# Optimization experiments

Measured on AMD Instinct MI355X. Metric: run time of the kernel, lower is better.

Reference implementation:

```python
import jax, jax.numpy as jnp
import numpy as np


def setup_inputs() -> dict:
    key = jax.random.key(0)
    kx, kw = jax.random.split(key)
    x = jax.random.normal(kx, (32, 2048, 256), dtype=jnp.float32)
    W = jax.random.normal(kw, (1024, 256), dtype=jnp.float32)  # codebook [K, D]
    return {"x": x, "W": W}


def reference(x, W):
    D = W.shape[1]
    flat = x.reshape(-1, D)  # [N, D]
    # Squared Euclidean distances [N, K]; argmin is identical to cdist argmin.
    d2 = (
        jnp.sum(flat * flat, axis=1, keepdims=True)
        - 2.0 * (flat @ W.T)
        + jnp.sum(W * W, axis=1)
    )
    idx = jnp.argmin(d2, axis=1)  # [N]
    quant = W[idx].reshape(x.shape)  # direct gather == one-hot @ W
    # Straight-through estimator
    quantized = x + jax.lax.stop_gradient(quant - x)
    e_latent = jnp.mean((jax.lax.stop_gradient(quantized) - x) ** 2)
    q_latent = jnp.mean((quantized - jax.lax.stop_gradient(x)) ** 2)
    commitment_cost = 0.25
    loss = q_latent + commitment_cost * e_latent
    return quantized, loss, idx[:, None]
```

## Files before the change

kernel.cpp:

```cpp
#include <hip/hip_runtime.h>


#define NROWS    65536
#define DDIM     256
#define KCODES   1024
#define DEXT     512
#define ND_TOTAL 16777216

typedef __attribute__((ext_vector_type(8))) short bf16x8;
typedef __attribute__((ext_vector_type(4))) float floatx4;

__device__ __forceinline__ unsigned short f2bf(float f) {
    unsigned int u = __float_as_uint(f);
    return (unsigned short)((u + 0x7FFFu + ((u >> 16) & 1u)) >> 16);
}
__device__ __forceinline__ float bf2f(unsigned short h) {
    return __uint_as_float((unsigned int)h << 16);
}
__device__ __forceinline__ void split4(float4 v, ushort4* hi, ushort4* lo) {
    unsigned short hx = f2bf(v.x), hy = f2bf(v.y), hz = f2bf(v.z), hw = f2bf(v.w);
    *hi = make_ushort4(hx, hy, hz, hw);
    *lo = make_ushort4(f2bf(v.x - bf2f(hx)), f2bf(v.y - bf2f(hy)),
                       f2bf(v.z - bf2f(hz)), f2bf(v.w - bf2f(hw)));
}
__device__ __forceinline__ void async_copy16(void* lds, const void* g) {
    __builtin_amdgcn_global_load_lds(
        (const __attribute__((address_space(1))) unsigned int*)g,
        (__attribute__((address_space(3))) unsigned int*)lds, 16, 0, 0);
}

__device__ __forceinline__ void merge2(float& v1, int& k1, float& v2, int& k2,
                                       float o1, int ok1, float o2, int ok2) {
    bool aw = (v1 < o1) || (v1 == o1 && k1 < ok1);
    float ca = aw ? v2 : v1; int kca = aw ? k2 : k1;
    float cb = aw ? o1 : o2; int kcb = aw ? ok1 : ok2;
    float nv1 = aw ? v1 : o1; int nk1 = aw ? k1 : ok1;
    bool cw = (ca < cb) || (ca == cb && kca < kcb);
    v1 = nv1; k1 = nk1;
    v2 = cw ? ca : cb; k2 = cw ? kca : kcb;
}

__global__ __launch_bounds__(256) void vq_prep(
    const float* __restrict__ x, unsigned short* __restrict__ Xhat,
    const float* __restrict__ W, unsigned short* __restrict__ What,
    float* __restrict__ w2, float* __restrict__ w2m, float* __restrict__ lossws)
{
    const int b = blockIdx.x;
    if (b < 16384) {
        int gid = b * 256 + threadIdx.x;
        int row = gid >> 6, q = gid & 63;
        float4 v = ((const float4*)x)[gid];
        ushort4 hv, lv;
        split4(v, &hv, &lv);
        unsigned short* r = Xhat + (size_t)row * DEXT;
        *(ushort4*)(r + q * 4) = hv;
        *(ushort4*)(r + 256 + q * 4) = lv;
    } else {
        int k = (b - 16384) * 256 + threadIdx.x;
        if (k == 0) lossws[0] = 0.0f;
        const float4* wr = (const float4*)(W + (size_t)k * DDIM);
        unsigned short* hrow = What + (size_t)k * DEXT;
        float s = 0.0f;
        for (int i = 0; i < 64; ++i) {
            float4 v = wr[i];
            s = fmaf(v.x, v.x, s); s = fmaf(v.y, v.y, s);
            s = fmaf(v.z, v.z, s); s = fmaf(v.w, v.w, s);
            ushort4 hv, lv;
            split4(v, &hv, &lv);
            *(ushort4*)(hrow + i * 4) = hv;
            *(ushort4*)(hrow + 256 + i * 4) = lv;
        }
        w2[k] = s;
        w2m[k] = s - 256.0f;
    }
}

__global__ __launch_bounds__(512, 2) void vq_main(
    const unsigned short* Xhat, const unsigned short* __restrict__ What,
    const float* __restrict__ x, const float* __restrict__ W,
    const float* __restrict__ w2, const float* __restrict__ w2m,
    float* qout, float* lossws, float* idx_out)
{
    __shared__ __align__(16) unsigned short smem[2 * 24576];
    __shared__ float Wm[KCODES];

    int*   rk1   = (int*)smem;
    int*   rk2   = rk1 + 512;
    int*   candk = rk2 + 512;
    float* resc  = (float*)(candk + 1024);
    int*   fink  = (int*)(resc + 1024);

    const int tid  = threadIdx.x;
    const int wave = tid >> 6, lane = tid & 63;
    const int quad = lane >> 4, l15 = lane & 15;
    const int wr = wave >> 2, wc = wave & 3;
    const int row0 = blockIdx.x * 128;

    Wm[tid] = w2m[tid];
    Wm[512 + tid] = w2m[512 + tid];

    float s1[16], s2[16];
    #pragma unroll
    for (int s = 0; s < 16; ++s) { s1[s] = 3.0e38f; s2[s] = 3.0e38f; }

    const int r0 = tid >> 2, p0 = tid & 3;
    const int psw = (p0 ^ ((r0 >> 1) & 3)) << 3;
    const int quadS8 = (quad ^ ((l15 >> 1) & 3)) << 3;
    const unsigned short* Ab = Xhat + (size_t)row0 * DEXT;

    auto STAGE = [&](int q, int cb) {
        const int ct = q >> 3, dc = (q & 7) << 5;
        const unsigned short* An = Ab + (size_t)r0 * DEXT + dc + psw;
        const unsigned short* Bn = What + ((size_t)(ct * 256 + r0)) * DEXT + dc + psw;
        unsigned short* L = smem + cb * 24576 + tid * 8;
        async_copy16(L,          An);
        async_copy16(L + 4096,   An + 256);
        async_copy16(L + 8192,   Bn);
        async_copy16(L + 12288,  Bn + 128 * DEXT);
        async_copy16(L + 16384,  Bn + 256);
        async_copy16(L + 20480,  Bn + 128 * DEXT + 256);
    };

    STAGE(0, 0);
    STAGE(1, 1);

    floatx4 acc[4][4];
    #pragma unroll
    for (int i = 0; i < 4; ++i)
        #pragma unroll
        for (int j = 0; j < 4; ++j) acc[i][j] = (floatx4){0.f, 0.f, 0.f, 0.f};

    #pragma unroll 1
    for (int q = 0; q < 32; ++q) {
        const int cb = q & 1;
        if (q != 31) { asm volatile("s_waitcnt vmcnt(6)" ::: "memory"); }
        else         { asm volatile("s_waitcnt vmcnt(0)" ::: "memory"); }
        __builtin_amdgcn_s_barrier();
        asm volatile("" ::: "memory");
        __builtin_amdgcn_s_setprio(1);

        const unsigned short* Sb = smem + cb * 24576;
        bf16x8 a0[4], a1[4], b0[4], b1[4];
        #pragma unroll
        for (int i = 0; i < 4; ++i) {
            const int ro = (wr * 64 + i * 16 + l15) * 32 + quadS8;
            a0[i] = *(const bf16x8*)(Sb + ro);
            a1[i] = *(const bf16x8*)(Sb + 4096 + ro);
        }
        #pragma unroll
        for (int j = 0; j < 4; ++j) {
            const int ro = (wc * 64 + j * 16 + l15) * 32 + quadS8;
            b0[j] = *(const bf16x8*)(Sb + 8192 + ro);
            b1[j] = *(const bf16x8*)(Sb + 16384 + ro);
        }
        #pragma unroll
        for (int i = 0; i < 4; ++i)
            #pragma unroll
            for (int j = 0; j < 4; ++j) {
                acc[i][j] = __builtin_amdgcn_mfma_f32_16x16x32_bf16(a0[i], b0[j], acc[i][j], 0, 0, 0);
                acc[i][j] = __builtin_amdgcn_mfma_f32_16x16x32_bf16(a1[i], b1[j], acc[i][j], 0, 0, 0);
                acc[i][j] = __builtin_amdgcn_mfma_f32_16x16x32_bf16(a0[i], b1[j], acc[i][j], 0, 0, 0);
                acc[i][j] = __builtin_amdgcn_mfma_f32_16x16x32_bf16(a1[i], b0[j], acc[i][j], 0, 0, 0);
            }
        __builtin_amdgcn_s_setprio(0);
        asm volatile("s_waitcnt lgkmcnt(0)" ::: "memory");
        __builtin_amdgcn_s_barrier();
        asm volatile("" ::: "memory");
        if (q + 2 < 32) STAGE(q + 2, cb);

        if ((q & 7) == 7) {
            const int ctf = q >> 3;
            #pragma unroll
            for (int j = 0; j < 4; ++j) {
                int cc = ctf * 256 + wc * 64 + j * 16 + l15;
                float wm = Wm[cc];
                unsigned pay = (unsigned)((j << 2) | ctf);
                #pragma unroll
                for (int i = 0; i < 4; ++i)
                    #pragma unroll
                    for (int r = 0; r < 4; ++r) {
                        float v = fmaf(-2.0f, acc[i][j][r], wm);
                        float pf = __uint_as_float((__float_as_uint(v) & 0xFFFFFFF0u) | pay);
                        int s = i * 4 + r;
                        float t = fminf(s1[s], pf);
                        s2[s] = fminf(s2[s], fmaxf(s1[s], pf));
                        s1[s] = t;
                    }
            }
            #pragma unroll
            for (int i = 0; i < 4; ++i)
                #pragma unroll
                for (int j = 0; j < 4; ++j) acc[i][j] = (floatx4){0.f, 0.f, 0.f, 0.f};
        }
    }

    float v1[16], v2[16];
    int k1[16], k2[16];
    #pragma unroll
    for (int s = 0; s < 16; ++s) {
        unsigned u1 = __float_as_uint(s1[s]) & 15u;
        unsigned u2 = __float_as_uint(s2[s]) & 15u;
        v1[s] = s1[s]; v2[s] = s2[s];
        k1[s] = (int)(u1 & 3u) * 256 + wc * 64 + (int)(u1 >> 2) * 16 + l15;
        k2[s] = (int)(u2 & 3u) * 256 + wc * 64 + (int)(u2 >> 2) * 16 + l15;
    }
    #pragma unroll
    for (int m = 1; m < 16; m <<= 1) {
        #pragma unroll
        for (int s = 0; s < 16; ++s) {
            float o1 = __shfl_xor(v1[s], m, 64);
            int  ok1 = __shfl_xor(k1[s], m, 64);
            float o2 = __shfl_xor(v2[s], m, 64);
            int  ok2 = __shfl_xor(k2[s], m, 64);
            merge2(v1[s], k1[s], v2[s], k2[s], o1, ok1, o2, ok2);
        }
    }
    if (l15 == 0) {
        #pragma unroll
        for (int s = 0; s < 16; ++s) {
            int row = wr * 64 + (s >> 2) * 16 + quad * 4 + (s & 3);
            rk1[wc * 128 + row] = k1[s];
            rk2[wc * 128 + row] = k2[s];
        }
    }
    __syncthreads();
    if (tid < 128) {
        #pragma unroll
        for (int h = 0; h < 4; ++h) {
            candk[tid * 8 + h * 2 + 0] = rk1[h * 128 + tid];
            candk[tid * 8 + h * 2 + 1] = rk2[h * 128 + tid];
        }
    }
    __syncthreads();
    #pragma unroll
    for (int j2 = 0; j2 < 2; ++j2) {
        int job = tid + j2 * 512;
        int r = job >> 3, cn = job & 7;
        int k = candk[r * 8 + cn];
        const float4* xr  = (const float4*)(x + (size_t)(row0 + r) * DDIM);
        const float4* wrp = (const float4*)(W + (size_t)k * DDIM);
        float dot = 0.0f;
        #pragma unroll 8
        for (int i = 0; i < 64; ++i) {
            float4 va = xr[i], vb = wrp[i];
            dot = fmaf(va.x, vb.x, dot); dot = fmaf(va.y, vb.y, dot);
            dot = fmaf(va.z, vb.z, dot); dot = fmaf(va.w, vb.w, dot);
        }
        resc[r * 8 + cn] = fmaf(-2.0f, dot, w2[k]);
    }
    __syncthreads();
    if (tid < 128) {
        float bd = resc[tid * 8 + 0];
        int   bk = candk[tid * 8 + 0];
        #pragma unroll
        for (int cn = 1; cn < 8; ++cn) {
            float d = resc[tid * 8 + cn];
            int   k = candk[tid * 8 + cn];
            if (d < bd || (d == bd && k < bk)) { bd = d; bk = k; }
        }
        fink[tid] = bk;
        idx_out[row0 + tid] = (float)bk;
    }
    __syncthreads();

    const int c4 = tid & 63, rsub = tid >> 6;
    float lsum = 0.0f;
    for (int it2 = 0; it2 < 16; ++it2) {
        int r = it2 * 8 + rsub;
        int k = fink[r];
        float4 wv = ((const float4*)(W + (size_t)k * DDIM))[c4];
        float4 xv = ((const float4*)(x + (size_t)(row0 + r) * DDIM))[c4];
        ((float4*)(qout + (size_t)(row0 + r) * DDIM))[c4] = wv;
        float dx = wv.x - xv.x, dy = wv.y - xv.y;
        float dz = wv.z - xv.z, dw = wv.w - xv.w;
        lsum = fmaf(dx, dx, lsum); lsum = fmaf(dy, dy, lsum);
        lsum = fmaf(dz, dz, lsum); lsum = fmaf(dw, dw, lsum);
    }
    #pragma unroll
    for (int off = 32; off > 0; off >>= 1) lsum += __shfl_down(lsum, off, 64);
    if (lane == 0) atomicAdd(lossws, lsum);
}

__global__ void vq_fin(const float* __restrict__ lossws, float* __restrict__ loss_out) {
    loss_out[0] = 1.25f * lossws[0] / (float)ND_TOTAL;
}

extern "C" void kernel_launch(void* const* d_in, const int* in_sizes, int n_in,
                              void* d_out, int out_size, void* d_ws, size_t ws_size,
                              hipStream_t stream) {
    const float* x = (const float*)d_in[0];
    const float* W = (const float*)d_in[1];
    float* out = (float*)d_out;
    unsigned short* Xhat = (unsigned short*)d_out;
    unsigned short* What = (unsigned short*)d_ws;
    float* w2     = (float*)((char*)d_ws + (1 << 20));
    float* w2m    = w2 + 1024;
    float* lossws = w2 + 2048;
    float* idx_out = out + (size_t)ND_TOTAL + 1;

    vq_prep<<<16388, 256, 0, stream>>>(x, Xhat, W, What, w2, w2m, lossws);
    vq_main<<<512, 512, 0, stream>>>(Xhat, What, x, W, w2, w2m, out, lossws, idx_out);
    vq_fin<<<1, 1, 0, stream>>>(lossws, out + ND_TOTAL);
}
```

Baseline: 405.1 us.

## Triple-buffer LDS stages and interleave split async copies with MFMA groups

Expands shared-memory staging from two to three buffers and splits each stage's global-to-LDS copies into three parts. The parts are issued between per-column MFMA groups, with extra barriers. The aim is to overlap loads with matrix math and remove the end-of-iteration wait-and-barrier bubble. Larger LDS use likely cuts blocks per CU, and the extra barriers add sync cost.

New measurement: 400.1 us. About the same (-1.2%).

```diff
diff --git a/kernel.cpp b/kernel.cpp
--- a/kernel.cpp
+++ b/kernel.cpp
@@ -81,7 +81,7 @@
     const float* __restrict__ w2, const float* __restrict__ w2m,
     float* qout, float* lossws, float* idx_out)
 {
-    __shared__ __align__(16) unsigned short smem[2 * 24576];
+    __shared__ __align__(16) unsigned short smem[3 * 24576];
     __shared__ float Wm[KCODES];
 
     int*   rk1   = (int*)smem;
@@ -108,21 +108,26 @@
     const int quadS8 = (quad ^ ((l15 >> 1) & 3)) << 3;
     const unsigned short* Ab = Xhat + (size_t)row0 * DEXT;
 
-    auto STAGE = [&](int q, int cb) {
+    auto STAGEP = [&](int q, int part) {
         const int ct = q >> 3, dc = (q & 7) << 5;
-        const unsigned short* An = Ab + (size_t)r0 * DEXT + dc + psw;
-        const unsigned short* Bn = What + ((size_t)(ct * 256 + r0)) * DEXT + dc + psw;
-        unsigned short* L = smem + cb * 24576 + tid * 8;
-        async_copy16(L,          An);
-        async_copy16(L + 4096,   An + 256);
-        async_copy16(L + 8192,   Bn);
-        async_copy16(L + 12288,  Bn + 128 * DEXT);
-        async_copy16(L + 16384,  Bn + 256);
-        async_copy16(L + 20480,  Bn + 128 * DEXT + 256);
+        unsigned short* L = smem + (q % 3) * 24576 + tid * 8;
+        if (part == 0) {
+            const unsigned short* An = Ab + (size_t)r0 * DEXT + dc + psw;
+            async_copy16(L,        An);
+            async_copy16(L + 4096, An + 256);
+        } else if (part == 1) {
+            const unsigned short* Bn = What + ((size_t)(ct * 256 + r0)) * DEXT + dc + psw;
+            async_copy16(L + 8192,  Bn);
+            async_copy16(L + 12288, Bn + 128 * DEXT);
+        } else {
+            const unsigned short* Bn = What + ((size_t)(ct * 256 + r0)) * DEXT + dc + psw;
+            async_copy16(L + 16384, Bn + 256);
+            async_copy16(L + 20480, Bn + 128 * DEXT + 256);
+        }
     };
 
-    STAGE(0, 0);
-    STAGE(1, 1);
+    STAGEP(0, 0); STAGEP(0, 1); STAGEP(0, 2);
+    STAGEP(1, 0); STAGEP(1, 1); STAGEP(1, 2);
 
     floatx4 acc[4][4];
     #pragma unroll
@@ -132,41 +137,51 @@
 
     #pragma unroll 1
     for (int q = 0; q < 32; ++q) {
-        const int cb = q & 1;
+        const unsigned short* Sb = smem + (q % 3) * 24576;
         if (q != 31) { asm volatile("s_waitcnt vmcnt(6)" ::: "memory"); }
         else         { asm volatile("s_waitcnt vmcnt(0)" ::: "memory"); }
+
+        bf16x8 a0[4], a1[4];
         __builtin_amdgcn_s_barrier();
         asm volatile("" ::: "memory");
-        __builtin_amdgcn_s_setprio(1);
-
-        const unsigned short* Sb = smem + cb * 24576;
-        bf16x8 a0[4], a1[4], b0[4], b1[4];
         #pragma unroll
         for (int i = 0; i < 4; ++i) {
             const int ro = (wr * 64 + i * 16 + l15) * 32 + quadS8;
             a0[i] = *(const bf16x8*)(Sb + ro);
             a1[i] = *(const bf16x8*)(Sb + 4096 + ro);
         }
-        #pragma unroll
-        for (int j = 0; j < 4; ++j) {
+        {
+            const int ro = (wc * 64 + 0 * 16 + l15) * 32 + quadS8;
+            bf16x8 b0 = *(const bf16x8*)(Sb + 8192 + ro);
+            bf16x8 b1 = *(const bf16x8*)(Sb + 16384 + ro);
+            __builtin_amdgcn_s_setprio(1);
+            #pragma unroll
+            for (int i = 0; i < 4; ++i) {
+                acc[i][0] = __builtin_amdgcn_mfma_f32_16x16x32_bf16(a0[i], b0, acc[i][0], 0, 0, 0);
+                acc[i][0] = __builtin_amdgcn_mfma_f32_16x16x32_bf16(a1[i], b1, acc[i][0], 0, 0, 0);
+                acc[i][0] = __builtin_amdgcn_mfma_f32_16x16x32_bf16(a0[i], b1, acc[i][0], 0, 0, 0);
+                acc[i][0] = __builtin_amdgcn_mfma_f32_16x16x32_bf16(a1[i], b0, acc[i][0], 0, 0, 0);
+            }
+            __builtin_amdgcn_s_setprio(0);
+        }
+        #pragma unroll
+        for (int j = 1; j < 4; ++j) {
+            __builtin_amdgcn_s_barrier();
+            asm volatile("" ::: "memory");
             const int ro = (wc * 64 + j * 16 + l15) * 32 + quadS8;
-            b0[j] = *(const bf16x8*)(Sb + 8192 + ro);
-            b1[j] = *(const bf16x8*)(Sb + 16384 + ro);
-        }
-        #pragma unroll
-        for (int i = 0; i < 4; ++i)
+            bf16x8 b0 = *(const bf16x8*)(Sb + 8192 + ro);
+            bf16x8 b1 = *(const bf16x8*)(Sb + 16384 + ro);
+            if (q + 2 < 32) STAGEP(q + 2, j - 1);
+            __builtin_amdgcn_s_setprio(1);
             #pragma unroll
-            for (int j = 0; j < 4; ++j) {
-                acc[i][j] = __builtin_amdgcn_mfma_f32_16x16x32_bf16(a0[i], b0[j], acc[i][j], 0, 0, 0);
-                acc[i][j] = __builtin_amdgcn_mfma_f32_16x16x32_bf16(a1[i], b1[j], acc[i][j], 0, 0, 0);
-                acc[i][j] = __builtin_amdgcn_mfma_f32_16x16x32_bf16(a0[i], b1[j], acc[i][j], 0, 0, 0);
-                acc[i][j] = __builtin_amdgcn_mfma_f32_16x16x32_bf16(a1[i], b0[j], acc[i][j], 0, 0, 0);
+            for (int i = 0; i < 4; ++i) {
+                acc[i][j] = __builtin_amdgcn_mfma_f32_16x16x32_bf16(a0[i], b0, acc[i][j], 0, 0, 0);
+                acc[i][j] = __builtin_amdgcn_mfma_f32_16x16x32_bf16(a1[i], b1, acc[i][j], 0, 0, 0);
+                acc[i][j] = __builtin_amdgcn_mfma_f32_16x16x32_bf16(a0[i], b1, acc[i][j], 0, 0, 0);
+                acc[i][j] = __builtin_amdgcn_mfma_f32_16x16x32_bf16(a1[i], b0, acc[i][j], 0, 0, 0);
             }
-        __builtin_amdgcn_s_setprio(0);
-        asm volatile("s_waitcnt lgkmcnt(0)" ::: "memory");
-        __builtin_amdgcn_s_barrier();
-        asm volatile("" ::: "memory");
-        if (q + 2 < 32) STAGE(q + 2, cb);
+            __builtin_amdgcn_s_setprio(0);
+        }
 
         if ((q & 7) == 7) {
             const int ctf = q >> 3;
```
